# Kernel optimization log

Hardware: AMD Instinct MI355X
Metric: run time of the kernel (lower is better)

## Reference

```python
import jax, jax.numpy as jnp
import numpy as np

B, T, C, H, HD = 2, 2048, 768, 12, 64


def setup_inputs() -> dict:
    key = jax.random.key(0)
    k0, k1, k2, k3 = jax.random.split(key, 4)
    x = jax.random.normal(k0, (B, T, C), dtype=jnp.float32)
    w_attn = jax.random.normal(k1, (3 * H * HD, C), dtype=jnp.float32) * 0.02
    b_attn = jnp.zeros((3 * H * HD,), dtype=jnp.float32)
    w_proj = jax.random.normal(k2, (C, H * HD), dtype=jnp.float32) * 0.02
    b_proj = jnp.zeros((C,), dtype=jnp.float32)
    sel_w = jax.random.normal(k3, (H,), dtype=jnp.float32) * 0.3
    return {"x": x, "w_attn": w_attn, "b_attn": b_attn,
            "w_proj": w_proj, "b_proj": b_proj, "sel_w": sel_w}


def reference(x, w_attn, b_attn, w_proj, b_proj, sel_w):
    Bc, Tc, Cc = x.shape
    Hc = sel_w.shape[0]
    HDc = w_attn.shape[0] // (3 * Hc)
    qkv = x @ w_attn.T + b_attn                          # [B,T,3*H*HD]
    q, k, v = jnp.split(qkv, 3, axis=2)
    q = q.reshape(Bc, Tc, Hc, HDc).transpose(0, 2, 1, 3)  # [B,H,T,HD]
    k = k.reshape(Bc, Tc, Hc, HDc).transpose(0, 2, 1, 3)
    v = v.reshape(Bc, Tc, Hc, HDc).transpose(0, 2, 1, 3)

    scale = 1.0 / np.sqrt(HDc).astype(np.float32)
    att = jnp.einsum('bhid,bhjd->bhij', q, k) * scale    # [B,H,T,T]
    causal = jnp.tril(jnp.ones((Tc, Tc), dtype=bool))
    neg_inf = jnp.asarray(-jnp.inf, dtype=att.dtype)
    att = jnp.where(causal[None, None], att, neg_inf)

    # selection head: per-head linear combo of (causally-zeroed) logits
    att0 = jnp.where(causal[None, None], att, 0.0)       # -inf -> 0 before combo
    S = jnp.einsum('bhij,h->bij', att0, sel_w)           # [B,T,T], bias=False
    S = jnp.where(causal[None], S, 0.0)
    S = jax.nn.relu(S)
    S = S.at[..., 0].set(0.0)                            # protect_bos_token
    S = S * (1.0 - jnp.eye(Tc, dtype=S.dtype))           # prevent_from_masking_myself

    FF = jnp.cumsum(S, axis=-2)                          # forgetting accumulation over rows
    FF_shifted = jnp.concatenate(
        [jnp.zeros_like(FF[..., :1, :]), FF[..., :-1, :]], axis=-2)

    att = jax.nn.softmax(att - FF_shifted[:, None], axis=-1)
    y = jnp.einsum('bhij,bhjd->bhid', att, v)            # [B,H,T,HD]
    y = y.transpose(0, 2, 1, 3).reshape(Bc, Tc, Hc * HDc)
    return y @ w_proj.T + b_proj
```

## Files before the change

### kernel.cpp

```cpp
#include <hip/hip_runtime.h>

#define B_   2
#define T_   2048
#define C_   768
#define H_   12
#define HD_  64
#define M_   (B_ * T_)
#define N3_  (3 * C_)
#define KB_  (C_ * 2)

typedef __bf16 bf16_t;
typedef bf16_t bf16x8 __attribute__((ext_vector_type(8)));
typedef float  floatx4 __attribute__((ext_vector_type(4)));
typedef unsigned long long u64_t;

__device__ inline floatx4 mfma_bf16(bf16x8 a, bf16x8 b, floatx4 c) {
    return __builtin_amdgcn_mfma_f32_16x16x32_bf16(a, b, c, 0, 0, 0);
}

__device__ __forceinline__ void async_copy16(const void* g, void* l) {
    __builtin_amdgcn_global_load_lds(
        (const __attribute__((address_space(1))) void*)g,
        (__attribute__((address_space(3))) void*)l, 16, 0, 0);
}

__device__ __forceinline__ bf16x8 frag_read(const char* ldsbase, int row, int quad) {
    int slot = quad ^ ((row >> 1) & 3);
    return *(const bf16x8*)(ldsbase + row * 64 + slot * 16);
}

template<bool TRIPLE>
__device__ __forceinline__ void gemm_loop8(
    const char* Ah, const char* Al, const char* Bh, const char* Bl,
    char* lds, floatx4 (&acc)[4][2])
{
    int tid = threadIdx.x, lane = tid & 63, wave = tid >> 6;
    int l15 = lane & 15, quad = lane >> 4;
    int wr = wave >> 2, wc = wave & 3;
    const int PH = TRIPLE ? 32768 : 16384;
    auto stage1 = [&](const char* tile, char* base, int k0) {
        int p = tid;
        int r = p >> 2, slot = p & 3;
        int g = slot ^ ((r >> 1) & 3);
        async_copy16(tile + (size_t)r * KB_ + k0 + g * 16, base + p * 16);
    };
    auto stage = [&](int ph, int k0) {
        char* base = lds + ph * PH;
        stage1(Ah, base, k0);
        stage1(Bh, base + 8192, k0);
        if (TRIPLE) {
            stage1(Al, base + 16384, k0);
            stage1(Bl, base + 24576, k0);
        }
    };
    stage(0, 0);
    int ph = 0;
#pragma unroll 1
    for (int k0 = 0; k0 < KB_; k0 += 64) {
        __syncthreads();
        if (k0 + 64 < KB_) stage(ph ^ 1, k0 + 64);
        char* base = lds + ph * PH;
        bf16x8 ah[4], al[4], bh[2], bl[2];
#pragma unroll
        for (int t = 0; t < 4; ++t) {
            ah[t] = frag_read(base, wr * 64 + t * 16 + l15, quad);
            if (TRIPLE)
                al[t] = frag_read(base + 16384, wr * 64 + t * 16 + l15, quad);
        }
#pragma unroll
        for (int t = 0; t < 2; ++t) {
            bh[t] = frag_read(base + 8192, wc * 32 + t * 16 + l15, quad);
            if (TRIPLE)
                bl[t] = frag_read(base + 24576, wc * 32 + t * 16 + l15, quad);
        }
#pragma unroll
        for (int mi = 0; mi < 4; ++mi)
#pragma unroll
            for (int ni = 0; ni < 2; ++ni) {
                acc[mi][ni] = mfma_bf16(ah[mi], bh[ni], acc[mi][ni]);
                if (TRIPLE) {
                    acc[mi][ni] = mfma_bf16(ah[mi], bl[ni], acc[mi][ni]);
                    acc[mi][ni] = mfma_bf16(al[mi], bh[ni], acc[mi][ni]);
                }
            }
        ph ^= 1;
    }
}

__global__ __launch_bounds__(256) void prep_kernel(
    const float* __restrict__ x, const float* __restrict__ w_attn,
    const float* __restrict__ w_proj,
    bf16_t* __restrict__ x_hi, bf16_t* __restrict__ x_lo,
    bf16_t* __restrict__ w_hi, bf16_t* __restrict__ w_lo,
    bf16_t* __restrict__ wp_b, int nx, int nw, int np)
{
    int gid = blockIdx.x * 256 + threadIdx.x;
    if (gid < nx) {
        float f = x[gid];
        bf16_t h = (bf16_t)f;
        x_hi[gid] = h;
        x_lo[gid] = (bf16_t)(f - (float)h);
    } else if (gid < nx + nw) {
        int i = gid - nx;
        float f = w_attn[i];
        bf16_t h = (bf16_t)f;
        w_hi[i] = h;
        w_lo[i] = (bf16_t)(f - (float)h);
    } else if (gid < nx + nw + np) {
        int i = gid - nx - nw;
        wp_b[i] = (bf16_t)w_proj[i];
    }
}

__global__ __launch_bounds__(512) void qkv_gemm(
    const bf16_t* __restrict__ x_hi, const bf16_t* __restrict__ x_lo,
    const bf16_t* __restrict__ w_hi, const bf16_t* __restrict__ w_lo,
    const float* __restrict__ bias, const float* __restrict__ selw,
    bf16_t* __restrict__ q_hi, bf16_t* __restrict__ q_lo,
    bf16_t* __restrict__ kw_hi, bf16_t* __restrict__ kw_lo,
    bf16_t* __restrict__ k_b, bf16_t* __restrict__ v_b)
{
    extern __shared__ char lds[];
    int m0 = blockIdx.x * 128, n0 = blockIdx.y * 128;
    floatx4 acc[4][2];
#pragma unroll
    for (int i = 0; i < 4; ++i)
#pragma unroll
        for (int j = 0; j < 2; ++j) acc[i][j] = (floatx4){0.f, 0.f, 0.f, 0.f};
    if (n0 >= 2 * C_) {
        gemm_loop8<false>((const char*)(x_hi + (size_t)m0 * C_), nullptr,
                          (const char*)(w_hi + (size_t)n0 * C_), nullptr, lds, acc);
    } else {
        gemm_loop8<true>((const char*)(x_hi + (size_t)m0 * C_),
                         (const char*)(x_lo + (size_t)m0 * C_),
                         (const char*)(w_hi + (size_t)n0 * C_),
                         (const char*)(w_lo + (size_t)n0 * C_), lds, acc);
    }

    int tid = threadIdx.x, lane = tid & 63, wave = tid >> 6;
    int l15 = lane & 15, quad = lane >> 4;
    int wr = wave >> 2, wc = wave & 3;
    int cb = n0 + wc * 32;
#pragma unroll
    for (int ni = 0; ni < 2; ++ni) {
        int col = cb + ni * 16 + l15;
        float bb = bias[col];
#pragma unroll
        for (int mi = 0; mi < 4; ++mi)
#pragma unroll
            for (int r = 0; r < 4; ++r) {
                int row = m0 + wr * 64 + mi * 16 + quad * 4 + r;
                float v = acc[mi][ni][r] + bb;
                if (cb < C_) {
                    float vs = v * 0.125f;
                    bf16_t h = (bf16_t)vs;
                    q_hi[(size_t)row * C_ + col] = h;
                    q_lo[(size_t)row * C_ + col] = (bf16_t)(vs - (float)h);
                } else if (cb < 2 * C_) {
                    int c2 = col - C_;
                    k_b[(size_t)row * C_ + c2] = (bf16_t)v;
                    float kw = v * selw[c2 >> 6];
                    bf16_t h = (bf16_t)kw;
                    kw_hi[(size_t)row * C_ + c2] = h;
                    kw_lo[(size_t)row * C_ + c2] = (bf16_t)(kw - (float)h);
                } else {
                    v_b[(size_t)row * C_ + (col - 2 * C_)] = (bf16_t)v;
                }
            }
    }
}

#define SEG_    16
#define SEGLEN_ (T_ / SEG_)

__global__ __launch_bounds__(512) void s_gemm(
    const bf16_t* __restrict__ q_hi, const bf16_t* __restrict__ q_lo,
    const bf16_t* __restrict__ kw_hi, const bf16_t* __restrict__ kw_lo,
    float* __restrict__ SF, float* __restrict__ segsum)
{
    extern __shared__ char lds[];
    int t = blockIdx.x, b = blockIdx.z;
    int it = (int)((sqrtf(8.f * t + 1.f) - 1.f) * 0.5f);
    while ((it + 1) * (it + 2) / 2 <= t) ++it;
    while (it * (it + 1) / 2 > t) --it;
    int jt = t - it * (it + 1) / 2;
    int i0 = it * 128, j0 = jt * 128;
    float* out = SF + (size_t)b * T_ * T_;

    floatx4 acc[4][2];
#pragma unroll
    for (int i = 0; i < 4; ++i)
#pragma unroll
        for (int j = 0; j < 2; ++j) acc[i][j] = (floatx4){0.f, 0.f, 0.f, 0.f};
    size_t arow = ((size_t)b * T_ + i0) * C_;
    size_t brow = ((size_t)b * T_ + j0) * C_;
    gemm_loop8<true>((const char*)(kw_hi + brow), (const char*)(kw_lo + brow),
                     (const char*)(q_hi + arow), (const char*)(q_lo + arow),
                     lds, acc);

    int tid = threadIdx.x, lane = tid & 63, wave = tid >> 6;
    int l15 = lane & 15, quad = lane >> 4;
    int wr = wave >> 2, wc = wave & 3;
    float rs[4][4];
#pragma unroll
    for (int mi = 0; mi < 4; ++mi)
#pragma unroll
        for (int r = 0; r < 4; ++r) rs[mi][r] = 0.f;
#pragma unroll
    for (int ni = 0; ni < 2; ++ni) {
        int i = i0 + wc * 32 + ni * 16 + l15;
#pragma unroll
        for (int mi = 0; mi < 4; ++mi)
#pragma unroll
            for (int r = 0; r < 4; ++r) {
                int j = j0 + wr * 64 + mi * 16 + quad * 4 + r;
                float s = acc[mi][ni][r];
                s = (j >= 1 && j < i) ? fmaxf(s, 0.f) : 0.f;
                out[(size_t)j * T_ + i] = s;
                rs[mi][r] += s;
            }
    }
#pragma unroll
    for (int mi = 0; mi < 4; ++mi)
#pragma unroll
        for (int r = 0; r < 4; ++r) {
#pragma unroll
            for (int d = 1; d < 16; d <<= 1)
                rs[mi][r] += __shfl_xor(rs[mi][r], d);
        }
    float* red = (float*)lds;
    if (l15 == 0) {
#pragma unroll
        for (int mi = 0; mi < 4; ++mi)
#pragma unroll
            for (int r = 0; r < 4; ++r)
                red[wc * 128 + wr * 64 + mi * 16 + quad * 4 + r] = rs[mi][r];
    }
    __syncthreads();
    if (tid < 128) {
        float ssum = red[tid] + red[128 + tid] + red[256 + tid] + red[384 + tid];
        segsum[((size_t)b * SEG_ + it) * T_ + j0 + tid] = ssum;
    }
}

__global__ __launch_bounds__(256) void scan_apply(
    float* __restrict__ SF, const float* __restrict__ segsum)
{
    int gid  = blockIdx.x * 256 + threadIdx.x;
    int j    = gid & (T_ - 1);
    int rest = gid >> 11;
    int seg  = rest & (SEG_ - 1);
    int b    = rest >> 4;
    if (seg * SEGLEN_ + SEGLEN_ - 1 < j) return;
    float run = 0.f;
    for (int s = 0; s < seg; ++s) {
        float v = (s * SEGLEN_ + SEGLEN_ - 1 <= j) ? 0.f
                : segsum[((size_t)b * SEG_ + s) * T_ + j];
        run += v;
    }
    float* col = SF + (size_t)b * T_ * T_ + (size_t)j * T_ + seg * SEGLEN_;
#pragma unroll 4
    for (int i = 0; i < SEGLEN_; ++i) {
        float s = col[i];
        s = (seg * SEGLEN_ + i > j) ? s : 0.f;
        col[i] = run;
        run += s;
    }
}

__global__ __launch_bounds__(256) void vt_kernel(
    const bf16_t* __restrict__ v_b, bf16_t* __restrict__ vt)
{
    __shared__ bf16_t tile[64][72];
    int t0 = blockIdx.x * 64, h = blockIdx.y, b = blockIdx.z;
    int tid = threadIdx.x;
    int r = tid >> 2, sl = tid & 3;
    const bf16_t* src = v_b + ((size_t)(b * T_ + t0 + r)) * C_ + h * HD_ + sl * 16;
    *(int4*)&tile[r][sl * 16]     = *(const int4*)src;
    *(int4*)&tile[r][sl * 16 + 8] = *(const int4*)(src + 8);
    __syncthreads();
    int hd = tid >> 2, q = tid & 3;
#pragma unroll
    for (int half = 0; half < 2; ++half) {
        int c0 = (q * 2 + half) * 8;
        union { int4 i4; bf16_t e[8]; } u;
#pragma unroll
        for (int kk = 0; kk < 8; ++kk) u.e[kk] = tile[c0 + kk][hd];
        *(int4*)(vt + ((size_t)(b * H_ + h) * HD_ + hd) * T_ + t0 + c0) = u.i4;
    }
}

__global__ __launch_bounds__(256) void attn_kernel(
    const bf16_t* __restrict__ q_b, const bf16_t* __restrict__ k_b,
    const bf16_t* __restrict__ vt_g, const float* __restrict__ FF,
    bf16_t* __restrict__ y_b, float* __restrict__ opart,
    float* __restrict__ lpart)
{
    extern __shared__ __align__(16) char lds[];
    char* KL = lds;
    char* VL = lds + 16384;
    char* PB = lds + 32768;

    int tid = threadIdx.x, lane = tid & 63, wave = tid >> 6;
    int l15 = lane & 15, quad = lane >> 4;
    int u = blockIdx.x & 15, g = blockIdx.x >> 4;
    int tile, jlo, jhi, half;
    bool split;
    if (g == 0)      { tile = 16 + u; jlo = 0;  jhi = 15;       half = 0; split = true;  }
    else if (g == 1) { tile = u;      jlo = 0;  jhi = u;        half = 0; split = false; }
    else             { tile = 31 - u; jlo = 16; jhi = 31 - u;   half = 1; split = true;  }
    int h = blockIdx.y, b = blockIdx.z;
    int i0w = tile * 64 + wave * 16;
    const floatx4 fzero = {0.f, 0.f, 0.f, 0.f};

    const bf16_t* qrow = q_b + ((size_t)b * T_ + i0w + l15) * C_ + h * HD_;
    bf16x8 qa0 = *(const bf16x8*)(qrow + quad * 8);
    bf16x8 qa1 = *(const bf16x8*)(qrow + 32 + quad * 8);

    const bf16_t* kbase = k_b + (size_t)b * T_ * C_ + h * HD_;
    const bf16_t* vbase = vt_g + (size_t)(b * H_ + h) * HD_ * T_;
    const float* fpr[4];
#pragma unroll
    for (int r = 0; r < 4; ++r)
        fpr[r] = FF + ((size_t)b * T_ + jlo * 64 + quad * 4 + r) * T_ + i0w + l15;

    auto stage = [&](int ph, int j0) {
#pragma unroll
        for (int i = 0; i < 2; ++i) {
            int p = (wave * 2 + i) * 64 + lane;
            int r = p >> 3, sp = p & 7, s = sp ^ (r & 7);
            async_copy16(kbase + (size_t)(j0 + r) * C_ + s * 8, KL + ph * 8192 + p * 16);
        }
#pragma unroll
        for (int i = 0; i < 2; ++i) {
            int p = (wave * 2 + i) * 64 + lane;
            int r = p >> 3, sp = p & 7, s = sp ^ (r & 7);
            async_copy16(vbase + (size_t)r * T_ + j0 + s * 8, VL + ph * 8192 + p * 16);
        }
    };

    float l_lane = 0.f;
    floatx4 O[4];
#pragma unroll
    for (int nt = 0; nt < 4; ++nt) O[nt] = fzero;

    stage(0, jlo * 64);
    int ph = 0;
#pragma unroll 1
    for (int jc = jlo; jc <= jhi; ++jc) {
        __syncthreads();
        if (jc < jhi) stage(ph ^ 1, (jc + 1) * 64);

        float ff[4][4];
#pragma unroll
        for (int r = 0; r < 4; ++r) {
#pragma unroll
            for (int s = 0; s < 4; ++s) ff[s][r] = fpr[r][(size_t)s * 16 * T_];
            fpr[r] += (size_t)64 * T_;
        }
        const char* KLp = KL + ph * 8192;
        floatx4 pc[4];
#pragma unroll
        for (int s = 0; s < 4; ++s) {
            int r = s * 16 + l15;
            bf16x8 k0 = *(const bf16x8*)&KLp[r * 128 + ((quad     ^ (r & 7)) * 16)];
            bf16x8 k1 = *(const bf16x8*)&KLp[r * 128 + (((quad+4) ^ (r & 7)) * 16)];
            floatx4 p = mfma_bf16(k0, qa0, fzero);
            pc[s] = mfma_bf16(k1, qa1, p);
        }
        bool diag = (jc * 64 + 63 > i0w);
        float p[4][4];
#pragma unroll
        for (int s = 0; s < 4; ++s)
#pragma unroll
            for (int r = 0; r < 4; ++r) {
                float lg = pc[s][r] - ff[s][r] - 20.f;
                if (diag) {
                    int i = i0w + l15;
                    int j = jc * 64 + s * 16 + quad * 4 + r;
                    lg = (j <= i) ? lg : -__builtin_inff();
                }
                p[s][r] = __expf(lg);
            }
#pragma unroll
        for (int s = 0; s < 4; ++s)
            l_lane += (p[s][0] + p[s][1]) + (p[s][2] + p[s][3]);

        char* Pw = PB + wave * 2176;
        int x = l15 & 7;
#pragma unroll
        for (int s = 0; s < 4; ++s) {
            union { bf16_t e[4]; u64_t v; } u4;
#pragma unroll
            for (int r = 0; r < 4; ++r) u4.e[r] = (bf16_t)p[s][r];
            int slot = (s * 4 + quad) ^ x;
            *(u64_t*)(Pw + l15 * 136 + slot * 8) = u4.v;
        }
        asm volatile("s_waitcnt lgkmcnt(0)" ::: "memory");
        bf16x8 pa0, pa1;
        {
            union { u64_t d[2]; bf16x8 f; } c0, c1;
            c0.d[0] = *(const u64_t*)(Pw + l15 * 136 + (((2 * quad)     ^ x) * 8));
            c0.d[1] = *(const u64_t*)(Pw + l15 * 136 + (((2 * quad + 1) ^ x) * 8));
            c1.d[0] = *(const u64_t*)(Pw + l15 * 136 + (((8 + 2 * quad)     ^ x) * 8));
            c1.d[1] = *(const u64_t*)(Pw + l15 * 136 + (((8 + 2 * quad + 1) ^ x) * 8));
            pa0 = c0.f;
            pa1 = c1.f;
        }
        const char* VLp = VL + ph * 8192;
#pragma unroll
        for (int nt = 0; nt < 4; ++nt) {
            int rv = nt * 16 + l15;
            bf16x8 v0 = *(const bf16x8*)&VLp[rv * 128 + ((quad     ^ (rv & 7)) * 16)];
            bf16x8 v1 = *(const bf16x8*)&VLp[rv * 128 + (((quad+4) ^ (rv & 7)) * 16)];
            O[nt] = mfma_bf16(pa0, v0, O[nt]);
            O[nt] = mfma_bf16(pa1, v1, O[nt]);
        }
        ph ^= 1;
    }

    l_lane += __shfl_xor(l_lane, 16);
    l_lane += __shfl_xor(l_lane, 32);

    if (!split) {
#pragma unroll
        for (int r = 0; r < 4; ++r) {
            float lv = __shfl(l_lane, quad * 4 + r);
            float inv = 1.f / lv;
            int i = i0w + quad * 4 + r;
#pragma unroll
            for (int nt = 0; nt < 4; ++nt)
                y_b[((size_t)b * T_ + i) * C_ + h * HD_ + nt * 16 + l15] =
                    (bf16_t)(O[nt][r] * inv);
        }
    } else {
        size_t ob = ((((size_t)(b * H_ + h) * 16 + (tile - 16)) * 2 + half) * 4096);
#pragma unroll
        for (int r = 0; r < 4; ++r) {
            int rl = wave * 16 + quad * 4 + r;
#pragma unroll
            for (int nt = 0; nt < 4; ++nt)
                opart[ob + (size_t)rl * 64 + nt * 16 + l15] = O[nt][r];
        }
        if (quad == 0) {
            size_t lb = (((size_t)(b * H_ + h) * 16 + (tile - 16)) * 2 + half) * 64;
            lpart[lb + wave * 16 + l15] = l_lane;
        }
    }
}

__global__ __launch_bounds__(256) void merge_kernel(
    const float* __restrict__ opart, const float* __restrict__ lpart,
    bf16_t* __restrict__ y_b)
{
    int tt = blockIdx.x, h = blockIdx.y, b = blockIdx.z;
    size_t b0 = (((size_t)(b * H_ + h) * 16 + tt) * 2) * 4096;
    size_t l0 = (((size_t)(b * H_ + h) * 16 + tt) * 2) * 64;
    int tile = 16 + tt;
#pragma unroll 4
    for (int e = threadIdx.x; e < 4096; e += 256) {
        int row = e >> 6, col = e & 63;
        float l = lpart[l0 + row] + lpart[l0 + 64 + row];
        float o = opart[b0 + e] + opart[b0 + 4096 + e];
        y_b[((size_t)b * T_ + tile * 64 + row) * C_ + h * HD_ + col] =
            (bf16_t)(o / l);
    }
}

__global__ __launch_bounds__(512) void proj_gemm(
    const bf16_t* __restrict__ y_b, const bf16_t* __restrict__ wp_b,
    const float* __restrict__ bias, float* __restrict__ out)
{
    extern __shared__ char lds[];
    int m0 = blockIdx.x * 128, n0 = blockIdx.y * 128;
    floatx4 acc[4][2];
#pragma unroll
    for (int i = 0; i < 4; ++i)
#pragma unroll
        for (int j = 0; j < 2; ++j) acc[i][j] = (floatx4){0.f, 0.f, 0.f, 0.f};
    gemm_loop8<false>((const char*)(y_b + (size_t)m0 * C_), nullptr,
                      (const char*)(wp_b + (size_t)n0 * C_), nullptr, lds, acc);

    int tid = threadIdx.x, lane = tid & 63, wave = tid >> 6;
    int l15 = lane & 15, quad = lane >> 4;
    int wr = wave >> 2, wc = wave & 3;
#pragma unroll
    for (int ni = 0; ni < 2; ++ni) {
        int col = n0 + wc * 32 + ni * 16 + l15;
        float bb = bias[col];
#pragma unroll
        for (int mi = 0; mi < 4; ++mi)
#pragma unroll
            for (int r = 0; r < 4; ++r)
                out[(size_t)(m0 + wr * 64 + mi * 16 + quad * 4 + r) * C_ + col] =
                    acc[mi][ni][r] + bb;
    }
}

extern "C" void kernel_launch(void* const* d_in, const int* in_sizes, int n_in,
                              void* d_out, int out_size, void* d_ws, size_t ws_size,
                              hipStream_t stream)
{
    const float* x      = (const float*)d_in[0];
    const float* w_attn = (const float*)d_in[1];
    const float* b_attn = (const float*)d_in[2];
    const float* w_proj = (const float*)d_in[3];
    const float* b_proj = (const float*)d_in[4];
    const float* sel_w  = (const float*)d_in[5];
    float* out = (float*)d_out;

    char* ws = (char*)d_ws;
    size_t off = 0;
    auto alloc = [&](size_t bytes) {
        void* p = ws + off;
        off += (bytes + 255) & ~(size_t)255;
        return p;
    };
    const size_t MC2 = (size_t)M_ * C_ * 2;
    bf16_t* q_hi   = (bf16_t*)alloc(MC2);
    bf16_t* kw_hi  = (bf16_t*)alloc(MC2);
    bf16_t* k_b    = (bf16_t*)alloc(MC2);
    bf16_t* y_b    = (bf16_t*)alloc(MC2);
    bf16_t* wp_b   = (bf16_t*)alloc((size_t)C_ * C_ * 2);
    float*  segsum = (float*)alloc((size_t)B_ * SEG_ * T_ * 4);
    char* dead_base = (char*)alloc(3 * MC2);
    bf16_t* q_lo  = (bf16_t*)dead_base;
    bf16_t* kw_lo = (bf16_t*)(dead_base + MC2);
    bf16_t* v_b   = (bf16_t*)(dead_base + 2 * MC2);
    float*  opart = (float*)dead_base;
    float*  lpart = (float*)(dead_base + (size_t)B_ * H_ * 16 * 2 * 4096 * 4);
    char* shared_base = (char*)alloc((size_t)B_ * T_ * T_ * 4);
    bf16_t* x_hi = (bf16_t*)shared_base;
    bf16_t* x_lo = (bf16_t*)(shared_base + MC2);
    bf16_t* w_hi = (bf16_t*)(shared_base + 2 * MC2);
    bf16_t* w_lo = (bf16_t*)(shared_base + 2 * MC2 + (size_t)N3_ * C_ * 2);
    float*  SF   = (float*)shared_base;
    bf16_t* vt   = kw_hi;

    int nx = M_ * C_, nw = N3_ * C_, np = C_ * C_;
    int ntot = nx + nw + np;
    prep_kernel<<<dim3((ntot + 255) / 256), 256, 0, stream>>>(
        x, w_attn, w_proj, x_hi, x_lo, w_hi, w_lo, wp_b, nx, nw, np);

    qkv_gemm<<<dim3(M_ / 128, N3_ / 128), 512, 65536, stream>>>(
        x_hi, x_lo, w_hi, w_lo, b_attn, sel_w,
        q_hi, q_lo, kw_hi, kw_lo, k_b, v_b);
    s_gemm<<<dim3(136, 1, B_), 512, 65536, stream>>>(
        q_hi, q_lo, kw_hi, kw_lo, SF, segsum);
    vt_kernel<<<dim3(T_ / 64, H_, B_), 256, 0, stream>>>(v_b, vt);
    scan_apply<<<dim3(B_ * SEG_ * T_ / 256), 256, 0, stream>>>(SF, segsum);
    attn_kernel<<<dim3(48, H_, B_), 256, 41472, stream>>>(
        q_hi, k_b, vt, SF, y_b, opart, lpart);
    merge_kernel<<<dim3(16, H_, B_), 256, 0, stream>>>(opart, lpart, y_b);
    proj_gemm<<<dim3(M_ / 128, C_ / 128), 512, 32768, stream>>>(y_b, wp_b, b_proj, out);
}
```

Before: 260.3 us.

## Load K and V tiles directly into registers instead of staging through LDS

The attention kernel stops double-buffering K and V chunks in shared memory with async global-to-LDS copies and block-wide barriers. Each wave now loads its K and V MFMA operands straight from global memory into registers every iteration, and shared memory shrinks to the per-wave P transpose buffer. This removes the __syncthreads per chunk and frees LDS for higher occupancy. In exchange all four waves load the same K/V data redundantly from global/L2, and there is no software prefetch to hide load latency.

```diff
diff --git a/kernel.cpp b/kernel.cpp
--- a/kernel.cpp
+++ b/kernel.cpp
@@ -296,10 +296,7 @@
     bf16_t* __restrict__ y_b, float* __restrict__ opart,
     float* __restrict__ lpart)
 {
-    extern __shared__ __align__(16) char lds[];
-    char* KL = lds;
-    char* VL = lds + 16384;
-    char* PB = lds + 32768;
+    __shared__ __align__(16) char PB[4][2176];
 
     int tid = threadIdx.x, lane = tid & 63, wave = tid >> 6;
     int l15 = lane & 15, quad = lane >> 4;
@@ -324,33 +321,20 @@
     for (int r = 0; r < 4; ++r)
         fpr[r] = FF + ((size_t)b * T_ + jlo * 64 + quad * 4 + r) * T_ + i0w + l15;
 
-    auto stage = [&](int ph, int j0) {
-#pragma unroll
-        for (int i = 0; i < 2; ++i) {
-            int p = (wave * 2 + i) * 64 + lane;
-            int r = p >> 3, sp = p & 7, s = sp ^ (r & 7);
-            async_copy16(kbase + (size_t)(j0 + r) * C_ + s * 8, KL + ph * 8192 + p * 16);
-        }
-#pragma unroll
-        for (int i = 0; i < 2; ++i) {
-            int p = (wave * 2 + i) * 64 + lane;
-            int r = p >> 3, sp = p & 7, s = sp ^ (r & 7);
-            async_copy16(vbase + (size_t)r * T_ + j0 + s * 8, VL + ph * 8192 + p * 16);
-        }
-    };
-
     float l_lane = 0.f;
     floatx4 O[4];
 #pragma unroll
     for (int nt = 0; nt < 4; ++nt) O[nt] = fzero;
 
-    stage(0, jlo * 64);
-    int ph = 0;
 #pragma unroll 1
     for (int jc = jlo; jc <= jhi; ++jc) {
-        __syncthreads();
-        if (jc < jhi) stage(ph ^ 1, (jc + 1) * 64);
-
+        bf16x8 ka0[4], ka1[4];
+#pragma unroll
+        for (int s = 0; s < 4; ++s) {
+            const bf16_t* kr = kbase + (size_t)(jc * 64 + s * 16 + l15) * C_;
+            ka0[s] = *(const bf16x8*)(kr + quad * 8);
+            ka1[s] = *(const bf16x8*)(kr + 32 + quad * 8);
+        }
         float ff[4][4];
 #pragma unroll
         for (int r = 0; r < 4; ++r) {
@@ -358,15 +342,19 @@
             for (int s = 0; s < 4; ++s) ff[s][r] = fpr[r][(size_t)s * 16 * T_];
             fpr[r] += (size_t)64 * T_;
         }
-        const char* KLp = KL + ph * 8192;
+        bf16x8 va0[4], va1[4];
+#pragma unroll
+        for (int nt = 0; nt < 4; ++nt) {
+            const bf16_t* vr = vbase + (size_t)(nt * 16 + l15) * T_ + jc * 64;
+            va0[nt] = *(const bf16x8*)(vr + quad * 8);
+            va1[nt] = *(const bf16x8*)(vr + 32 + quad * 8);
+        }
+
         floatx4 pc[4];
 #pragma unroll
         for (int s = 0; s < 4; ++s) {
-            int r = s * 16 + l15;
-            bf16x8 k0 = *(const bf16x8*)&KLp[r * 128 + ((quad     ^ (r & 7)) * 16)];
-            bf16x8 k1 = *(const bf16x8*)&KLp[r * 128 + (((quad+4) ^ (r & 7)) * 16)];
-            floatx4 p = mfma_bf16(k0, qa0, fzero);
-            pc[s] = mfma_bf16(k1, qa1, p);
+            floatx4 p = mfma_bf16(ka0[s], qa0, fzero);
+            pc[s] = mfma_bf16(ka1[s], qa1, p);
         }
         bool diag = (jc * 64 + 63 > i0w);
         float p[4][4];
@@ -386,7 +374,7 @@
         for (int s = 0; s < 4; ++s)
             l_lane += (p[s][0] + p[s][1]) + (p[s][2] + p[s][3]);
 
-        char* Pw = PB + wave * 2176;
+        char* Pw = PB[wave];
         int x = l15 & 7;
 #pragma unroll
         for (int s = 0; s < 4; ++s) {
@@ -407,16 +395,11 @@
             pa0 = c0.f;
             pa1 = c1.f;
         }
-        const char* VLp = VL + ph * 8192;
 #pragma unroll
         for (int nt = 0; nt < 4; ++nt) {
-            int rv = nt * 16 + l15;
-            bf16x8 v0 = *(const bf16x8*)&VLp[rv * 128 + ((quad     ^ (rv & 7)) * 16)];
-            bf16x8 v1 = *(const bf16x8*)&VLp[rv * 128 + (((quad+4) ^ (rv & 7)) * 16)];
-            O[nt] = mfma_bf16(pa0, v0, O[nt]);
-            O[nt] = mfma_bf16(pa1, v1, O[nt]);
-        }
-        ph ^= 1;
+            O[nt] = mfma_bf16(pa0, va0[nt], O[nt]);
+            O[nt] = mfma_bf16(pa1, va1[nt], O[nt]);
+        }
     }
 
     l_lane += __shfl_xor(l_lane, 16);
@@ -549,7 +532,7 @@
         q_hi, q_lo, kw_hi, kw_lo, SF, segsum);
     vt_kernel<<<dim3(T_ / 64, H_, B_), 256, 0, stream>>>(v_b, vt);
     scan_apply<<<dim3(B_ * SEG_ * T_ / 256), 256, 0, stream>>>(SF, segsum);
-    attn_kernel<<<dim3(48, H_, B_), 256, 41472, stream>>>(
+    attn_kernel<<<dim3(48, H_, B_), 256, 0, stream>>>(
         q_hi, k_b, vt, SF, y_b, opart, lpart);
     merge_kernel<<<dim3(16, H_, B_), 256, 0, stream>>>(opart, lpart, y_b);
     proj_gemm<<<dim3(M_ / 128, C_ / 128), 512, 32768, stream>>>(y_b, wp_b, b_proj, out);
```

New measurement: 332.8 us. +27.9%, slower.
